# Kernel optimization log

Hardware: AMD Instinct MI355X
Metric: run time of the kernel (lower is better)

## Reference

```python
import jax, jax.numpy as jnp
import numpy as np

D = 512      # d_model
H = 8        # num_heads
DH = D // H  # d_head = 64
WIN = 10     # window_size
DFF = 2048   # d_ff
EPS = 1e-5   # LayerNorm eps


def _layernorm(x, w, b):
    mu = jnp.mean(x, axis=-1, keepdims=True)
    var = jnp.mean(jnp.square(x - mu), axis=-1, keepdims=True)
    return (x - mu) * jax.lax.rsqrt(var + EPS) * w + b


def setup_inputs() -> dict:
    key = jax.random.key(0)
    ks = jax.random.split(key, 8)
    s = 0.02
    inp = {
        "z": jax.random.normal(ks[0], (4, 2048, D), jnp.float32),
        "Wq": jax.random.normal(ks[1], (D, D), jnp.float32) * s,
        "bq": jnp.zeros((D,), jnp.float32),
        "Wk": jax.random.normal(ks[2], (D, D), jnp.float32) * s,
        "bk": jnp.zeros((D,), jnp.float32),
        "Wv": jax.random.normal(ks[3], (D, D), jnp.float32) * s,
        "bv": jnp.zeros((D,), jnp.float32),
        "Wo": jax.random.normal(ks[4], (D, D), jnp.float32) * s,
        "bo": jnp.zeros((D,), jnp.float32),
        "ln1_w": jnp.ones((D,), jnp.float32),
        "ln1_b": jnp.zeros((D,), jnp.float32),
        "W1": jax.random.normal(ks[5], (D, DFF), jnp.float32) * s,
        "b1": jnp.zeros((DFF,), jnp.float32),
        "W2": jax.random.normal(ks[6], (DFF, D), jnp.float32) * s,
        "b2": jnp.zeros((D,), jnp.float32),
        "ln2_w": jnp.ones((D,), jnp.float32),
        "ln2_b": jnp.zeros((D,), jnp.float32),
    }
    return inp


def reference(z, Wq, bq, Wk, bk, Wv, bv, Wo, bo, ln1_w, ln1_b, W1, b1, W2, b2, ln2_w, ln2_b):
    B, T, Dm = z.shape
    # projections -> [B, H, T, DH]
    q = (z @ Wq + bq).reshape(B, T, H, DH).transpose(0, 2, 1, 3)
    k = (z @ Wk + bk).reshape(B, T, H, DH).transpose(0, 2, 1, 3)
    v = (z @ Wv + bv).reshape(B, T, H, DH).transpose(0, 2, 1, 3)
    scale = 1.0 / jnp.sqrt(jnp.asarray(DH, z.dtype))
    scores = jnp.einsum('bhqd,bhkd->bhqk', q, k) * scale  # [B,H,T,T]
    idx = jnp.arange(T)
    dist = idx[:, None] - idx[None, :]
    valid = (dist >= 0) & (dist < WIN)
    neg = jnp.finfo(scores.dtype).min
    scores = jnp.where(valid[None, None], scores, neg)
    attn = jax.nn.softmax(scores, axis=-1)  # dropout is identity in eval
    out = jnp.einsum('bhqk,bhkd->bhqd', attn, v)
    out = out.transpose(0, 2, 1, 3).reshape(B, T, Dm)
    out = out @ Wo + bo
    z = _layernorm(z + out, ln1_w, ln1_b)
    # FFN with exact (erf) GELU, matching torch nn.GELU default
    ff = jax.nn.gelu(z @ W1 + b1, approximate=False) @ W2 + b2
    z = _layernorm(z + ff, ln2_w, ln2_b)
    return z
```

## Files before the change

kernel.cpp:

```cpp
#include <hip/hip_runtime.h>
#include <cstdint>
#include <cstddef>

#define DEV __device__ __forceinline__

typedef __bf16 bf16x8 __attribute__((ext_vector_type(8)));
typedef float f32x4 __attribute__((ext_vector_type(4)));
typedef unsigned short us8 __attribute__((ext_vector_type(8)));
typedef unsigned short us4 __attribute__((ext_vector_type(4)));

typedef const __attribute__((address_space(1))) unsigned int GUI;
typedef __attribute__((address_space(3))) unsigned int LUI;

DEV unsigned short f2bf(float f) {
  unsigned int u = __builtin_bit_cast(unsigned int, f);
  u += 0x7fffu + ((u >> 16) & 1u);
  return (unsigned short)(u >> 16);
}
DEV float bf2f(unsigned short h) {
  unsigned int u = ((unsigned int)h) << 16;
  return __builtin_bit_cast(float, u);
}

__global__ void k_f32_to_bf16(const float* __restrict__ in, unsigned short* __restrict__ out, int n4) {
  int i = blockIdx.x * blockDim.x + threadIdx.x;
  if (i >= n4) return;
  float4 v = ((const float4*)in)[i];
  us4 o;
  o.x = f2bf(v.x); o.y = f2bf(v.y); o.z = f2bf(v.z); o.w = f2bf(v.w);
  *(us4*)(out + (size_t)i * 4) = o;
}

__global__ void k_transpose_bf16(const float* __restrict__ in, unsigned short* __restrict__ out,
                                 int K, int N) {
  __shared__ float tile[32][33];
  int n0 = blockIdx.x * 32, k0 = blockIdx.y * 32;
  int tx = threadIdx.x, ty = threadIdx.y;
#pragma unroll
  for (int i = 0; i < 32; i += 8)
    tile[ty + i][tx] = in[(size_t)(k0 + ty + i) * N + n0 + tx];
  __syncthreads();
#pragma unroll
  for (int i = 0; i < 32; i += 8)
    out[(size_t)(n0 + ty + i) * K + k0 + tx] = f2bf(tile[tx][ty + i]);
}

__global__ void k_transpose4(const float* __restrict__ p0, const float* __restrict__ p1,
                             const float* __restrict__ p2, const float* __restrict__ p3,
                             unsigned short* __restrict__ base) {
  __shared__ float tile[32][33];
  const float* in = blockIdx.z == 0 ? p0 : blockIdx.z == 1 ? p1 : blockIdx.z == 2 ? p2 : p3;
  unsigned short* out = base + (size_t)blockIdx.z * 262144;
  int n0 = blockIdx.x * 32, k0 = blockIdx.y * 32;
  int tx = threadIdx.x, ty = threadIdx.y;
#pragma unroll
  for (int i = 0; i < 32; i += 8)
    tile[ty + i][tx] = in[(size_t)(k0 + ty + i) * 512 + n0 + tx];
  __syncthreads();
#pragma unroll
  for (int i = 0; i < 32; i += 8)
    out[(size_t)(n0 + ty + i) * 512 + k0 + tx] = f2bf(tile[tx][ty + i]);
}

__global__ void k_concat_bias(const float* __restrict__ bq, const float* __restrict__ bk,
                              const float* __restrict__ bv, float* __restrict__ out) {
  int i = blockIdx.x * blockDim.x + threadIdx.x;
  float v = (i < 512) ? bq[i] : (i < 1024 ? bk[i - 512] : bv[i - 1024]);
  out[i] = v;
}

template <int MODE, int SPLITK>
DEV void gemm_body(const unsigned short* __restrict__ A,
                   const unsigned short* __restrict__ BT,
                   const float* __restrict__ bias,
                   unsigned short* __restrict__ outp,
                   int K, int N) {
  __shared__ __align__(16) unsigned short As[2 * 16384];
  __shared__ __align__(16) unsigned short Bs[2 * 16384];
  const int tid = threadIdx.x;
  const int wave = tid >> 6, lane = tid & 63;
  const int wm = wave >> 2, wn = wave & 3;

  const int nx = gridDim.x, ny = gridDim.y;
  const int nwg = nx * ny * SPLITK;
  const int lid = (blockIdx.z * ny + blockIdx.y) * nx + blockIdx.x;
  const int q8 = nwg >> 3, r8 = nwg & 7;
  const int xcd = lid & 7, slot = lid >> 3;
  const int wid = (xcd < r8 ? xcd * (q8 + 1) : r8 * (q8 + 1) + (xcd - r8) * q8) + slot;
  const int nbz = nx * SPLITK;
  const int bxz = wid % nbz;
  const int by  = wid / nbz;
  const int bx  = bxz % nx;
  const int z   = bxz / nx;

  const int rbase = by * 256;
  const int nbase = bx * 256;
  const int nkt = (K / SPLITK) >> 6;
  const int kb = z * (K / SPLITK);

  float bv_[4];
#pragma unroll
  for (int n = 0; n < 4; ++n) {
    int gcol = nbase + wn * 64 + n * 16 + (lane & 15);
    bv_[n] = (z == 0) ? bias[gcol] : 0.f;
  }
  asm volatile("s_waitcnt vmcnt(0)" ::: "memory");

  auto STAGE = [&](int buf, int k0) {
#pragma unroll
    for (int t = 0; t < 4; ++t) {
      int s = t * 512 + tid;
      int row = s >> 3;
      int col = ((s & 7) ^ (row & 7)) << 3;
      const unsigned short* ga = A + (size_t)(rbase + row) * K + k0 + col;
      const unsigned short* gb = BT + (size_t)(nbase + row) * K + k0 + col;
      const int dst = buf * 16384 + (t * 512 + wave * 64) * 8;
      __builtin_amdgcn_global_load_lds((GUI*)ga, (LUI*)(As + dst), 16, 0, 0);
      __builtin_amdgcn_global_load_lds((GUI*)gb, (LUI*)(Bs + dst), 16, 0, 0);
    }
  };

  f32x4 acc[8][4] = {};
  STAGE(0, kb);

  for (int kt = 0; kt < nkt; ++kt) {
    const int cur = kt & 1;
    if (kt + 1 < nkt) {
      STAGE(cur ^ 1, kb + (kt + 1) * 64);
      asm volatile("s_waitcnt vmcnt(8)" ::: "memory");
    } else {
      asm volatile("s_waitcnt vmcnt(0)" ::: "memory");
    }
    __builtin_amdgcn_s_barrier();

#pragma unroll
    for (int ks = 0; ks < 2; ++ks) {
      bf16x8 af[8], bfr[4];
#pragma unroll
      for (int m = 0; m < 8; ++m) {
        int row = wm * 128 + m * 16 + (lane & 15);
        int ch = (ks * 4 + (lane >> 4)) ^ (row & 7);
        af[m] = __builtin_bit_cast(bf16x8, *(const us8*)(As + cur * 16384 + row * 64 + ch * 8));
      }
#pragma unroll
      for (int n = 0; n < 4; ++n) {
        int row = wn * 64 + n * 16 + (lane & 15);
        int ch = (ks * 4 + (lane >> 4)) ^ (row & 7);
        bfr[n] = __builtin_bit_cast(bf16x8, *(const us8*)(Bs + cur * 16384 + row * 64 + ch * 8));
      }
      __builtin_amdgcn_s_setprio(1);
#pragma unroll
      for (int m = 0; m < 8; ++m)
#pragma unroll
        for (int n = 0; n < 4; ++n)
          acc[m][n] = __builtin_amdgcn_mfma_f32_16x16x32_bf16(af[m], bfr[n], acc[m][n], 0, 0, 0);
      __builtin_amdgcn_s_setprio(0);
    }
    asm volatile("s_waitcnt lgkmcnt(0)" ::: "memory");
    __builtin_amdgcn_s_barrier();
  }

  unsigned short* opv = outp + (size_t)z * 8192 * N;
#pragma unroll
  for (int m = 0; m < 8; ++m) {
    int grow0 = rbase + wm * 128 + m * 16 + ((lane >> 4) << 2);
#pragma unroll
    for (int n = 0; n < 4; ++n) {
      int gcol = nbase + wn * 64 + n * 16 + (lane & 15);
#pragma unroll
      for (int r = 0; r < 4; ++r) {
        float v = acc[m][n][r] + bv_[n];
        if (MODE == 2) v = 0.5f * v * (1.0f + erff(v * 0.70710678118654752f));
        opv[(size_t)(grow0 + r) * N + gcol] = f2bf(v);
      }
    }
  }
}

__global__ __launch_bounds__(512) void k_qkv(const unsigned short* __restrict__ A,
                                             const unsigned short* __restrict__ BT,
                                             const float* __restrict__ bias,
                                             unsigned short* __restrict__ outp, int K, int N) {
  gemm_body<0, 1>(A, BT, bias, outp, K, N);
}
__global__ __launch_bounds__(512) void k_wo(const unsigned short* __restrict__ A,
                                            const unsigned short* __restrict__ BT,
                                            const float* __restrict__ bias,
                                            unsigned short* __restrict__ outp, int K, int N) {
  gemm_body<0, 4>(A, BT, bias, outp, K, N);
}
__global__ __launch_bounds__(512) void k_ffn1(const unsigned short* __restrict__ A,
                                              const unsigned short* __restrict__ BT,
                                              const float* __restrict__ bias,
                                              unsigned short* __restrict__ outp, int K, int N) {
  gemm_body<2, 1>(A, BT, bias, outp, K, N);
}
__global__ __launch_bounds__(512) void k_ffn2(const unsigned short* __restrict__ A,
                                              const unsigned short* __restrict__ BT,
                                              const float* __restrict__ bias,
                                              unsigned short* __restrict__ outp, int K, int N) {
  gemm_body<0, 4>(A, BT, bias, outp, K, N);
}

__global__ __launch_bounds__(64) void k_attn(const unsigned short* __restrict__ qkv,
                                             unsigned short* __restrict__ attnb) {
  __shared__ float Qt[64 * 67];
  __shared__ float Kt[64 * 75];
  __shared__ float P[64 * 12];

  const int lane = threadIdx.x;
  const int bid = blockIdx.x;
  const int chunk = bid & 31;
  const int bh = bid >> 5;
  const int h = bh & 7, b = bh >> 3;
  const int i0 = chunk * 64;
  const int b2048 = b * 2048;
  const int h64 = h * 64;

#pragma unroll 8
  for (int r = 0; r < 73; ++r) {
    int jloc = i0 - 9 + r;
    int jc = jloc < 0 ? 0 : jloc;
    Kt[lane * 75 + r] = bf2f(qkv[(size_t)(b2048 + jc) * 1536 + 512 + h64 + lane]);
  }
#pragma unroll 8
  for (int r = 0; r < 64; ++r) {
    Qt[lane * 67 + r] = bf2f(qkv[(size_t)(b2048 + i0 + r) * 1536 + h64 + lane]);
  }
  __syncthreads();

  float s[10];
#pragma unroll
  for (int jj = 0; jj < 10; ++jj) s[jj] = 0.f;
#pragma unroll
  for (int d = 0; d < 64; ++d) {
    float qd = Qt[d * 67 + lane];
#pragma unroll
    for (int jj = 0; jj < 10; ++jj)
      s[jj] = fmaf(qd, Kt[d * 75 + lane + jj], s[jj]);
  }
  const int iG = i0 + lane;
#pragma unroll
  for (int jj = 0; jj < 10; ++jj)
    s[jj] = (iG - 9 + jj >= 0) ? s[jj] * 0.125f : -1e30f;
  float mx = s[9];
#pragma unroll
  for (int jj = 0; jj < 9; ++jj) mx = fmaxf(mx, s[jj]);
  float den = 0.f;
#pragma unroll
  for (int jj = 0; jj < 10; ++jj) {
    s[jj] = __expf(s[jj] - mx);
    den += s[jj];
  }
  float inv = 1.f / den;
#pragma unroll
  for (int jj = 0; jj < 10; ++jj) P[lane * 12 + jj] = s[jj] * inv;
  __syncthreads();

  for (int q0 = 0; q0 < 64; q0 += 4) {
    float vv[13];
#pragma unroll
    for (int t = 0; t < 13; ++t) {
      int jloc = i0 + q0 - 9 + t;
      int jc = jloc < 0 ? 0 : jloc;
      vv[t] = bf2f(qkv[(size_t)(b2048 + jc) * 1536 + 1024 + h64 + lane]);
    }
#pragma unroll
    for (int qq = 0; qq < 4; ++qq) {
      const int q = q0 + qq;
      const float* pp = &P[q * 12];
      float o = 0.f;
#pragma unroll
      for (int jj = 0; jj < 10; ++jj) o = fmaf(pp[jj], vv[qq + jj], o);
      attnb[(size_t)(b2048 + i0 + q) * 512 + h64 + lane] = f2bf(o);
    }
  }
}

template <int V, int NP>
DEV void ln_body(const void* __restrict__ resv,
                 const unsigned short* __restrict__ add,
                 const float* __restrict__ w,
                 const float* __restrict__ bb,
                 void* __restrict__ outp) {
  const size_t PLANE = (size_t)8192 * 512;
  const int wave = threadIdx.x >> 6, lane = threadIdx.x & 63;
  const int row = blockIdx.x * 4 + wave;
  float x[8];
  if (V == 0) {
    const float4* r4 = (const float4*)((const float*)resv + (size_t)row * 512) + lane * 2;
    float4 a = r4[0], b = r4[1];
    x[0] = a.x; x[1] = a.y; x[2] = a.z; x[3] = a.w;
    x[4] = b.x; x[5] = b.y; x[6] = b.z; x[7] = b.w;
  } else {
    us8 r = *(const us8*)((const unsigned short*)resv + (size_t)row * 512 + lane * 8);
#pragma unroll
    for (int j = 0; j < 8; ++j) x[j] = bf2f(r[j]);
  }
#pragma unroll
  for (int p = 0; p < NP; ++p) {
    us8 a = *(const us8*)(add + p * PLANE + (size_t)row * 512 + lane * 8);
#pragma unroll
    for (int j = 0; j < 8; ++j) x[j] += bf2f(a[j]);
  }
  float sum = 0.f, ss = 0.f;
#pragma unroll
  for (int j = 0; j < 8; ++j) {
    sum += x[j];
    ss += x[j] * x[j];
  }
#pragma unroll
  for (int m = 32; m >= 1; m >>= 1) {
    sum += __shfl_xor(sum, m);
    ss += __shfl_xor(ss, m);
  }
  const float mu = sum * (1.f / 512.f);
  float var = ss * (1.f / 512.f) - mu * mu;
  const float rstd = rsqrtf(var + 1e-5f);
  const int c = lane * 8;
  float o[8];
#pragma unroll
  for (int j = 0; j < 8; ++j) o[j] = (x[j] - mu) * rstd * w[c + j] + bb[c + j];
  if (V == 0) {
    us8 u;
#pragma unroll
    for (int j = 0; j < 8; ++j) u[j] = f2bf(o[j]);
    *(us8*)((unsigned short*)outp + (size_t)row * 512 + c) = u;
  } else {
    float4 u0, u1;
    u0.x = o[0]; u0.y = o[1]; u0.z = o[2]; u0.w = o[3];
    u1.x = o[4]; u1.y = o[5]; u1.z = o[6]; u1.w = o[7];
    float4* o4 = (float4*)((float*)outp + (size_t)row * 512 + c);
    o4[0] = u0; o4[1] = u1;
  }
}

__global__ __launch_bounds__(256) void k_ln_mid(const float* __restrict__ res,
                                                const unsigned short* __restrict__ add,
                                                const float* __restrict__ w,
                                                const float* __restrict__ bb,
                                                unsigned short* __restrict__ outp) {
  ln_body<0, 4>(res, add, w, bb, outp);
}
__global__ __launch_bounds__(256) void k_ln_out(const unsigned short* __restrict__ res,
                                                const unsigned short* __restrict__ add,
                                                const float* __restrict__ w,
                                                const float* __restrict__ bb,
                                                float* __restrict__ outp) {
  ln_body<1, 4>(res, add, w, bb, outp);
}

extern "C" void kernel_launch(void* const* d_in, const int* in_sizes, int n_in,
                              void* d_out, int out_size, void* d_ws, size_t ws_size,
                              hipStream_t stream) {
  const float* z    = (const float*)d_in[0];
  const float* Wq   = (const float*)d_in[1];
  const float* bq   = (const float*)d_in[2];
  const float* Wk   = (const float*)d_in[3];
  const float* bk   = (const float*)d_in[4];
  const float* Wv   = (const float*)d_in[5];
  const float* bv   = (const float*)d_in[6];
  const float* Wo   = (const float*)d_in[7];
  const float* bo   = (const float*)d_in[8];
  const float* ln1w = (const float*)d_in[9];
  const float* ln1b = (const float*)d_in[10];
  const float* W1   = (const float*)d_in[11];
  const float* b1   = (const float*)d_in[12];
  const float* W2   = (const float*)d_in[13];
  const float* b2   = (const float*)d_in[14];
  const float* ln2w = (const float*)d_in[15];
  const float* ln2b = (const float*)d_in[16];
  float* out = (float*)d_out;

  char* ws = (char*)d_ws;
  size_t off = 0;
  auto alloc = [&](size_t bytes) {
    char* p = ws + off;
    off += (bytes + 255) & ~(size_t)255;
    return p;
  };
  unsigned short* Wsq   = (unsigned short*)alloc((size_t)2048 * 512 * 2);
  unsigned short* WTqkv = Wsq;
  unsigned short* WoT   = Wsq + (size_t)1536 * 512;
  unsigned short* W1T   = (unsigned short*)alloc((size_t)2048 * 512 * 2);
  unsigned short* W2T   = (unsigned short*)alloc((size_t)512 * 2048 * 2);
  float*          biasqkv = (float*)alloc(1536 * 4);
  unsigned short* zb    = (unsigned short*)alloc((size_t)8192 * 512 * 2);
  unsigned short* qkvb  = (unsigned short*)alloc((size_t)8192 * 1536 * 2);
  unsigned short* attnb = (unsigned short*)alloc((size_t)8192 * 512 * 2);
  unsigned short* p1    = (unsigned short*)alloc((size_t)4 * 8192 * 512 * 2);
  unsigned short* z1b   = zb;
  unsigned short* ff    = qkvb;

  dim3 tb(32, 8);
  k_f32_to_bf16<<<4096, 256, 0, stream>>>(z, zb, 1048576);
  k_transpose4<<<dim3(16, 16, 4), tb, 0, stream>>>(Wq, Wk, Wv, Wo, Wsq);
  k_transpose_bf16<<<dim3(64, 16), tb, 0, stream>>>(W1, W1T, 512, 2048);
  k_transpose_bf16<<<dim3(16, 64), tb, 0, stream>>>(W2, W2T, 2048, 512);
  k_concat_bias<<<6, 256, 0, stream>>>(bq, bk, bv, biasqkv);

  k_qkv<<<dim3(6, 32), 512, 0, stream>>>(zb, WTqkv, biasqkv, qkvb, 512, 1536);
  k_attn<<<1024, 64, 0, stream>>>(qkvb, attnb);
  k_wo<<<dim3(2, 32, 4), 512, 0, stream>>>(attnb, WoT, bo, p1, 512, 512);
  k_ln_mid<<<2048, 256, 0, stream>>>(z, p1, ln1w, ln1b, z1b);
  k_ffn1<<<dim3(8, 32), 512, 0, stream>>>(z1b, W1T, b1, ff, 512, 2048);
  k_ffn2<<<dim3(2, 32, 4), 512, 0, stream>>>(ff, W2T, b2, p1, 2048, 512);
  k_ln_out<<<2048, 256, 0, stream>>>(z1b, p1, ln2w, ln2b, out);
}
```

Baseline: 151.5 us.

## Deepen GEMM pipeline to four-stage 32-wide K tiles with pair-row swizzle

The shared GEMM body moves from a double-buffered 64-wide K tile to a four-slot ring of 32-wide K tiles, keeping three tiles in flight with graded vmcnt waits. The LDS layout packs two 32-element row halves into each 64-element line under a new XOR swizzle, and all fragment reads are issued before a sched_barrier that separates them from the MFMA block. The aim is to hide global-load latency with deeper prefetch at the same LDS footprint. In exchange there are twice as many barrier-synchronised iterations, each with half the MFMA work to amortise them.

```diff
diff --git a/kernel.cpp b/kernel.cpp
--- a/kernel.cpp
+++ b/kernel.cpp
@@ -75,18 +75,19 @@
                    const float* __restrict__ bias,
                    unsigned short* __restrict__ outp,
                    int K, int N) {
-  __shared__ __align__(16) unsigned short As[2 * 16384];
-  __shared__ __align__(16) unsigned short Bs[2 * 16384];
+  __shared__ __align__(16) unsigned short As[4 * 8192];
+  __shared__ __align__(16) unsigned short Bs[4 * 8192];
   const int tid = threadIdx.x;
   const int wave = tid >> 6, lane = tid & 63;
   const int wm = wave >> 2, wn = wave & 3;
+  const int q = lane >> 4, l15 = lane & 15;
 
   const int nx = gridDim.x, ny = gridDim.y;
   const int nwg = nx * ny * SPLITK;
   const int lid = (blockIdx.z * ny + blockIdx.y) * nx + blockIdx.x;
   const int q8 = nwg >> 3, r8 = nwg & 7;
-  const int xcd = lid & 7, slot = lid >> 3;
-  const int wid = (xcd < r8 ? xcd * (q8 + 1) : r8 * (q8 + 1) + (xcd - r8) * q8) + slot;
+  const int xcd = lid & 7, slot0 = lid >> 3;
+  const int wid = (xcd < r8 ? xcd * (q8 + 1) : r8 * (q8 + 1) + (xcd - r8) * q8) + slot0;
   const int nbz = nx * SPLITK;
   const int bxz = wid % nbz;
   const int by  = wid / nbz;
@@ -95,26 +96,29 @@
 
   const int rbase = by * 256;
   const int nbase = bx * 256;
-  const int nkt = (K / SPLITK) >> 6;
-  const int kb = z * (K / SPLITK);
+  const int kper = K / SPLITK;
+  const int nkt = kper >> 5;
+  const int kb = z * kper;
 
   float bv_[4];
 #pragma unroll
   for (int n = 0; n < 4; ++n) {
-    int gcol = nbase + wn * 64 + n * 16 + (lane & 15);
+    int gcol = nbase + wn * 64 + n * 16 + l15;
     bv_[n] = (z == 0) ? bias[gcol] : 0.f;
   }
   asm volatile("s_waitcnt vmcnt(0)" ::: "memory");
 
-  auto STAGE = [&](int buf, int k0) {
-#pragma unroll
-    for (int t = 0; t < 4; ++t) {
-      int s = t * 512 + tid;
-      int row = s >> 3;
-      int col = ((s & 7) ^ (row & 7)) << 3;
-      const unsigned short* ga = A + (size_t)(rbase + row) * K + k0 + col;
-      const unsigned short* gb = BT + (size_t)(nbase + row) * K + k0 + col;
-      const int dst = buf * 16384 + (t * 512 + wave * 64) * 8;
+  auto STAGE = [&](int slot, int k0) {
+#pragma unroll
+    for (int i = 0; i < 2; ++i) {
+      int s = i * 512 + tid;
+      int R = s >> 3;
+      int c = (s & 7) ^ (R & 7);
+      int r = 2 * R + (c >> 2);
+      int kl = (c & 3) << 3;
+      const unsigned short* ga = A + (size_t)(rbase + r) * K + k0 + kl;
+      const unsigned short* gb = BT + (size_t)(nbase + r) * K + k0 + kl;
+      const int dst = slot * 8192 + (i * 512 + wave * 64) * 8;
       __builtin_amdgcn_global_load_lds((GUI*)ga, (LUI*)(As + dst), 16, 0, 0);
       __builtin_amdgcn_global_load_lds((GUI*)gb, (LUI*)(Bs + dst), 16, 0, 0);
     }
@@ -122,51 +126,58 @@
 
   f32x4 acc[8][4] = {};
   STAGE(0, kb);
-
-  for (int kt = 0; kt < nkt; ++kt) {
-    const int cur = kt & 1;
-    if (kt + 1 < nkt) {
-      STAGE(cur ^ 1, kb + (kt + 1) * 64);
+  STAGE(1, kb + 32);
+  STAGE(2, kb + 64);
+
+  for (int t = 0; t < nkt; ++t) {
+    if (t + 3 < nkt) {
+      STAGE((t + 3) & 3, kb + (t + 3) * 32);
+      asm volatile("s_waitcnt vmcnt(12)" ::: "memory");
+    } else if (t + 2 < nkt) {
       asm volatile("s_waitcnt vmcnt(8)" ::: "memory");
+    } else if (t + 1 < nkt) {
+      asm volatile("s_waitcnt vmcnt(4)" ::: "memory");
     } else {
       asm volatile("s_waitcnt vmcnt(0)" ::: "memory");
     }
     __builtin_amdgcn_s_barrier();
 
-#pragma unroll
-    for (int ks = 0; ks < 2; ++ks) {
-      bf16x8 af[8], bfr[4];
-#pragma unroll
-      for (int m = 0; m < 8; ++m) {
-        int row = wm * 128 + m * 16 + (lane & 15);
-        int ch = (ks * 4 + (lane >> 4)) ^ (row & 7);
-        af[m] = __builtin_bit_cast(bf16x8, *(const us8*)(As + cur * 16384 + row * 64 + ch * 8));
-      }
-#pragma unroll
-      for (int n = 0; n < 4; ++n) {
-        int row = wn * 64 + n * 16 + (lane & 15);
-        int ch = (ks * 4 + (lane >> 4)) ^ (row & 7);
-        bfr[n] = __builtin_bit_cast(bf16x8, *(const us8*)(Bs + cur * 16384 + row * 64 + ch * 8));
-      }
-      __builtin_amdgcn_s_setprio(1);
-#pragma unroll
-      for (int m = 0; m < 8; ++m)
-#pragma unroll
-        for (int n = 0; n < 4; ++n)
-          acc[m][n] = __builtin_amdgcn_mfma_f32_16x16x32_bf16(af[m], bfr[n], acc[m][n], 0, 0, 0);
-      __builtin_amdgcn_s_setprio(0);
+    const unsigned short* Ab = As + (t & 3) * 8192;
+    const unsigned short* Bb = Bs + (t & 3) * 8192;
+    bf16x8 af[8], bfr[4];
+#pragma unroll
+    for (int m = 0; m < 8; ++m) {
+      int rr = wm * 128 + m * 16 + l15;
+      int R = rr >> 1;
+      int d = (((rr & 1) << 2) + q) ^ (R & 7);
+      af[m] = __builtin_bit_cast(bf16x8, *(const us8*)(Ab + R * 64 + d * 8));
+    }
+#pragma unroll
+    for (int n = 0; n < 4; ++n) {
+      int rr = wn * 64 + n * 16 + l15;
+      int R = rr >> 1;
+      int d = (((rr & 1) << 2) + q) ^ (R & 7);
+      bfr[n] = __builtin_bit_cast(bf16x8, *(const us8*)(Bb + R * 64 + d * 8));
     }
     asm volatile("s_waitcnt lgkmcnt(0)" ::: "memory");
+    __builtin_amdgcn_sched_barrier(0);
+    __builtin_amdgcn_s_setprio(1);
+#pragma unroll
+    for (int m = 0; m < 8; ++m)
+#pragma unroll
+      for (int n = 0; n < 4; ++n)
+        acc[m][n] = __builtin_amdgcn_mfma_f32_16x16x32_bf16(af[m], bfr[n], acc[m][n], 0, 0, 0);
+    __builtin_amdgcn_s_setprio(0);
     __builtin_amdgcn_s_barrier();
   }
 
   unsigned short* opv = outp + (size_t)z * 8192 * N;
 #pragma unroll
   for (int m = 0; m < 8; ++m) {
-    int grow0 = rbase + wm * 128 + m * 16 + ((lane >> 4) << 2);
+    int grow0 = rbase + wm * 128 + m * 16 + (q << 2);
 #pragma unroll
     for (int n = 0; n < 4; ++n) {
-      int gcol = nbase + wn * 64 + n * 16 + (lane & 15);
+      int gcol = nbase + wn * 64 + n * 16 + l15;
 #pragma unroll
       for (int r = 0; r < 4; ++r) {
         float v = acc[m][n][r] + bv_[n];
```

Measured after the change: 162.8 us. 7.4% more time.
